# Optimization experiments

Hardware: AMD Instinct MI355X
Metric: run time of the kernel (lower is better)

The kernel has to match this reference:

```python
import jax, jax.numpy as jnp
import numpy as np

WS = 512   # window_size
LB = 1     # look_backward
LF = 1     # look_forward
H = 16     # num_attention_heads
NC = LB + LF + 1  # concatenated windows per query window


def _collect(a, pad_value):
    # a: [B, nw, ws, ...]; gather windows [i-LB, i+LF] for each window i,
    # padding the window axis with pad_value (faithful to collect_windows).
    nw = a.shape[1]
    pads = [(0, 0), (LB, LF)] + [(0, 0)] * (a.ndim - 2)
    ap = jnp.pad(a, pads, constant_values=pad_value)
    idx = jnp.arange(nw)[:, None] + jnp.arange(NC)[None, :]  # [nw, NC]
    g = ap[:, idx]  # [B, nw, NC, ws, ...]
    return g.reshape(g.shape[0], nw, NC * a.shape[2], *a.shape[3:])


def setup_inputs() -> dict:
    key = jax.random.key(0)
    ks = jax.random.split(key, 9)
    B, S, E = 1, 4096, 1024
    x = jax.random.normal(ks[0], (B, S, E), dtype=jnp.float32)
    std = 0.02
    wq = std * jax.random.normal(ks[1], (E, E), dtype=jnp.float32)
    wk = std * jax.random.normal(ks[2], (E, E), dtype=jnp.float32)
    wv = std * jax.random.normal(ks[3], (E, E), dtype=jnp.float32)
    wo = std * jax.random.normal(ks[4], (E, E), dtype=jnp.float32)
    bq = std * jax.random.normal(ks[5], (E,), dtype=jnp.float32)
    bk = std * jax.random.normal(ks[6], (E,), dtype=jnp.float32)
    bv = std * jax.random.normal(ks[7], (E,), dtype=jnp.float32)
    bo = std * jax.random.normal(ks[8], (E,), dtype=jnp.float32)
    return {"x": x, "wq": wq, "bq": bq, "wk": wk, "bk": bk,
            "wv": wv, "bv": bv, "wo": wo, "bo": bo}


def reference(x, wq, bq, wk, bk, wv, bv, wo, bo):
    B, S, E = x.shape
    hd = E // H
    nw = S // WS  # seq_len chosen divisible by window_size

    def proj(w, b):
        y = x @ w.T + b
        return y.reshape(B, S, H, hd).transpose(0, 2, 1, 3).reshape(B * H, S, hd)

    q = proj(wq, bq)
    k = proj(wk, bk)
    v = proj(wv, bv)

    qb = q.reshape(B * H, nw, WS, hd)
    # NOTE: original pads K/V window buffers with value -1 (not zero); pad
    # positions are NOT masked (the `!= -1` clause excludes them) -- replicated.
    kb = _collect(k.reshape(B * H, nw, WS, hd), -1.0)  # [BH, nw, NC*WS, hd]
    vb = _collect(v.reshape(B * H, nw, WS, hd), -1.0)

    t = jnp.arange(S, dtype=jnp.int32).reshape(1, nw, WS)
    ct = _collect(t, -1)  # [1, nw, NC*WS] key positions (-1 for pads)

    # Unscaled QK^T (original applies no 1/sqrt(d)).
    scores = jnp.einsum('bwqd,bwkd->bwqk', qb, kb)  # [BH, nw, WS, NC*WS]

    qi = t.reshape(1, nw, WS, 1)          # query absolute positions
    ctb = ct[:, :, None, :]               # key absolute positions
    over = ((ctb > qi + WS * LF) | (ctb < qi - WS * LB)) & (ctb != -1)
    scores = jnp.where(over, -jnp.inf, scores)

    attn = jax.nn.softmax(scores, axis=-1)
    out = jnp.einsum('bwqk,bwkd->bwqd', attn, vb)  # [BH, nw, WS, hd]
    out = out.reshape(B, H, S, hd).transpose(0, 2, 1, 3).reshape(B, S, E)
    return out @ wo.T + bo
```

## Files before the change

### kernel.cpp

```cpp
#include <hip/hip_runtime.h>
#include <stdint.h>

#define S 4096
#define E 1024
#define NH 16
#define HD 64
#define WSZ 512

typedef _Float16 f16x8 __attribute__((ext_vector_type(8)));
typedef _Float16 f16x4 __attribute__((ext_vector_type(4)));
typedef float f32x4 __attribute__((ext_vector_type(4)));
typedef unsigned short u16;
typedef unsigned int u32;

__device__ __forceinline__ u16 f2h_bits(float f) {
    union { _Float16 h; u16 u; } cv; cv.h = (_Float16)f; return cv.u;
}

__device__ __forceinline__ void gld16(const u16* g, u16* l) {
    __builtin_amdgcn_global_load_lds((const __attribute__((address_space(1))) void*)g,
                                     (__attribute__((address_space(3))) void*)l, 16, 0, 0);
}

struct CvtArgs {
    const float* s[5];
    u16* d[5];
    int n[5];
};
__global__ void cvt5(CvtArgs a) {
    int seg = blockIdx.y;
    const float* __restrict__ s = a.s[seg];
    u16* __restrict__ d = a.d[seg];
    int n = a.n[seg];
    for (int i = (blockIdx.x * 256 + threadIdx.x) * 4; i < n; i += gridDim.x * 1024) {
        float4 f = *(const float4*)&s[i];
        uint2 o;
        o.x = (u32)f2h_bits(f.x) | ((u32)f2h_bits(f.y) << 16);
        o.y = (u32)f2h_bits(f.z) | ((u32)f2h_bits(f.w) << 16);
        *(uint2*)&d[i] = o;
    }
}

__global__ __launch_bounds__(256) void gemm_qkv(
    const u16* __restrict__ A, const u16* __restrict__ B,
    u16* __restrict__ OutQK, u16* __restrict__ OutVT,
    const float* __restrict__ b0, const float* __restrict__ b1, const float* __restrict__ b2,
    int K) {
    __shared__ __align__(16) u16 As[128 * 32];
    __shared__ __align__(16) u16 Bs[128 * 32];
    const int tid = threadIdx.x;
    const int wid = tid >> 6, lid = tid & 63, quad = lid >> 4, l16 = lid & 15;
    const int wm = wid >> 1, wn = wid & 1;
    const int bm0 = blockIdx.x * 128, bn0 = blockIdx.y * 128;

    f32x4 acc[4][4] = {};
    const int sr = tid >> 2, sc = (tid & 3) * 8;

    for (int k0 = 0; k0 < K; k0 += 32) {
        __syncthreads();
        gld16(&A[(size_t)(bm0 + sr) * K + k0 + sc],      &As[tid * 8]);
        gld16(&A[(size_t)(bm0 + sr + 64) * K + k0 + sc], &As[2048 + tid * 8]);
        gld16(&B[(size_t)(bn0 + sr) * K + k0 + sc],      &Bs[tid * 8]);
        gld16(&B[(size_t)(bn0 + sr + 64) * K + k0 + sc], &Bs[2048 + tid * 8]);
        __syncthreads();
        f16x8 af[4], bf[4];
#pragma unroll
        for (int i = 0; i < 4; ++i) af[i] = *(const f16x8*)&As[(wm * 64 + i * 16 + l16) * 32 + quad * 8];
#pragma unroll
        for (int j = 0; j < 4; ++j) bf[j] = *(const f16x8*)&Bs[(wn * 64 + j * 16 + l16) * 32 + quad * 8];
#pragma unroll
        for (int i = 0; i < 4; ++i)
#pragma unroll
            for (int j = 0; j < 4; ++j)
                acc[i][j] = __builtin_amdgcn_mfma_f32_16x16x32_f16(af[i], bf[j], acc[i][j], 0, 0, 0);
    }

    const bool isV = (bn0 >= 2048);
#pragma unroll
    for (int j = 0; j < 4; ++j) {
        int n = bn0 + wn * 64 + j * 16 + l16;
        float bias = (n < 1024) ? b0[n] : (n < 2048 ? b1[n - 1024] : b2[n - 2048]);
#pragma unroll
        for (int i = 0; i < 4; ++i) {
            int m0 = bm0 + wm * 64 + i * 16 + quad * 4;
            if (!isV) {
#pragma unroll
                for (int r = 0; r < 4; ++r)
                    OutQK[(size_t)(m0 + r) * 2048 + n] = f2h_bits(acc[i][j][r] + bias);
            } else {
                u16 h0 = f2h_bits(acc[i][j][0] + bias);
                u16 h1 = f2h_bits(acc[i][j][1] + bias);
                u16 h2 = f2h_bits(acc[i][j][2] + bias);
                u16 h3 = f2h_bits(acc[i][j][3] + bias);
                uint2 pk;
                pk.x = (u32)h0 | ((u32)h1 << 16);
                pk.y = (u32)h2 | ((u32)h3 << 16);
                *(uint2*)&OutVT[(size_t)(n - 2048) * 4096 + m0] = pk;
            }
        }
    }
}

__global__ __launch_bounds__(256) void gemm_n64(
    const u16* __restrict__ A, const u16* __restrict__ B, float* __restrict__ OutF,
    const float* __restrict__ bias, int N, int K) {
    __shared__ __align__(16) u16 As[128 * 32];
    __shared__ __align__(16) u16 Bs[64 * 32];
    const int tid = threadIdx.x;
    const int wid = tid >> 6, lid = tid & 63, quad = lid >> 4, l16 = lid & 15;
    const int bm0 = blockIdx.x * 128, bn0 = blockIdx.y * 64;

    f32x4 acc[2][4] = {};
    const int sr = tid >> 2, sc = (tid & 3) * 8;

    for (int k0 = 0; k0 < K; k0 += 32) {
        __syncthreads();
        gld16(&A[(size_t)(bm0 + sr) * K + k0 + sc],      &As[tid * 8]);
        gld16(&A[(size_t)(bm0 + sr + 64) * K + k0 + sc], &As[2048 + tid * 8]);
        gld16(&B[(size_t)(bn0 + sr) * K + k0 + sc],      &Bs[tid * 8]);
        __syncthreads();
        f16x8 af[2], bf[4];
#pragma unroll
        for (int i = 0; i < 2; ++i) af[i] = *(const f16x8*)&As[(wid * 32 + i * 16 + l16) * 32 + quad * 8];
#pragma unroll
        for (int j = 0; j < 4; ++j) bf[j] = *(const f16x8*)&Bs[(j * 16 + l16) * 32 + quad * 8];
#pragma unroll
        for (int i = 0; i < 2; ++i)
#pragma unroll
            for (int j = 0; j < 4; ++j)
                acc[i][j] = __builtin_amdgcn_mfma_f32_16x16x32_f16(af[i], bf[j], acc[i][j], 0, 0, 0);
    }

#pragma unroll
    for (int j = 0; j < 4; ++j) {
        int n = bn0 + j * 16 + l16;
        float bv = bias[n];
#pragma unroll
        for (int i = 0; i < 2; ++i) {
            int m0 = bm0 + wid * 32 + i * 16 + quad * 4;
#pragma unroll
            for (int r = 0; r < 4; ++r)
                OutF[(size_t)(m0 + r) * N + n] = acc[i][j][r] + bv;
        }
    }
}

__global__ __launch_bounds__(512, 4) void attn_win(const u16* __restrict__ QK, const u16* __restrict__ VT,
                                                   u16* __restrict__ AO) {
    const int qt = blockIdx.x, w = blockIdx.y, h = blockIdx.z;
    const int tid = threadIdx.x, wid = tid >> 6, lid = tid & 63, quad = lid >> 4, l16 = lid & 15;

    __shared__ __align__(16) u16 Ks[2][2 * 64 * 32];
    __shared__ __align__(16) u16 Vt[2][2 * 64 * 36];

    const int qrow = w * WSZ + qt * 128 + wid * 16 + l16;
    const _Float16 L2E = (_Float16)1.44269504f;
    f16x8 qf[2];
#pragma unroll
    for (int ks = 0; ks < 2; ++ks) {
        qf[ks] = *(const f16x8*)&QK[(size_t)qrow * 2048 + h * 64 + ks * 32 + quad * 8];
#pragma unroll
        for (int j = 0; j < 8; ++j) qf[ks][j] *= L2E;
    }

    const int npad = (w == 0 || w == 7) ? 512 : 0;
    float s_p = 0.f;
    if (npad) {
        float sq = 0.f;
#pragma unroll
        for (int j = 0; j < 8; ++j) sq += (float)qf[0][j] + (float)qf[1][j];
        sq += __shfl_xor(sq, 16, 64);
        sq += __shfl_xor(sq, 32, 64);
        s_p = -sq;
    }

    f32x4 oacc[4] = {};
    float mrun = -30000.f;
    float lsum = 0.f;

    const int g0base = (w - 1) * WSZ;
    const int rqloc = qt * 128 + wid * 16 + l16;
    const int rqw0 = qt * 128 + wid * 16;

    int cfirst = 2 * qt; if ((1 - w) * 8 > cfirst) cfirst = (1 - w) * 8;
    int clast = 2 * qt + 17; if (71 - 8 * w < clast) clast = 71 - 8 * w; if (clast > 23) clast = 23;

    const int kst = tid & 255, kkh = tid >> 8;
    const int vd = tid >> 3, vk0 = (tid & 7) * 8;
    const size_t kgoff = 1024 + h * 64 + kkh * 32 + (kst & 3) * 8 + (size_t)(kst >> 2) * 2048;
    const int kloff = kkh * 2048 + kst * 8;
    const u16* vgrow = VT + (size_t)(h * 64 + vd) * 4096 + vk0;
    const int vloff = (vk0 >> 5) * 2304 + vd * 36 + (vk0 & 31);

    {
        const int g0 = g0base + cfirst * 64;
        uint4 va = *(const uint4*)(vgrow + g0);
        gld16(QK + (size_t)g0 * 2048 + kgoff, &Ks[0][0] + kloff);
        u16* vp = &Vt[0][0] + vloff;
        *(uint2*)(vp)     = make_uint2(va.x, va.y);
        *(uint2*)(vp + 4) = make_uint2(va.z, va.w);
    }

    int ib = 0;
    for (int c = cfirst; c <= clast; ++c, ib ^= 1) {
        __syncthreads();

        const bool has_next = (c < clast);
        uint4 vnext;
        if (has_next) {
            const int gn = g0base + (c + 1) * 64;
            vnext = *(const uint4*)(vgrow + gn);
            gld16(QK + (size_t)gn * 2048 + kgoff, &Ks[ib ^ 1][0] + kloff);
        }

        const u16* KsB = &Ks[ib][0];
        const u16* VtB = &Vt[ib][0];

        f32x4 sc[4];
#pragma unroll
        for (int nt = 0; nt < 4; ++nt) {
            f16x8 kf0 = *(const f16x8*)&KsB[(nt * 16 + l16) * 32 + quad * 8];
            f16x8 kf1 = *(const f16x8*)&KsB[2048 + (nt * 16 + l16) * 32 + quad * 8];
            f32x4 t = {};
            t = __builtin_amdgcn_mfma_f32_16x16x32_f16(kf0, qf[0], t, 0, 0, 0);
            t = __builtin_amdgcn_mfma_f32_16x16x32_f16(kf1, qf[1], t, 0, 0, 0);
            sc[nt] = t;
        }

        const bool needs_mask = (c * 64 < rqw0 + 16) || (c * 64 + 63 > rqw0 + 1024);
        if (needs_mask) {
#pragma unroll
            for (int nt = 0; nt < 4; ++nt)
#pragma unroll
                for (int r = 0; r < 4; ++r) {
                    int n = c * 64 + nt * 16 + quad * 4 + r;
                    if (n < rqloc || n > rqloc + 1024) sc[nt][r] = -30000.f;
                }
        }

        float mloc = mrun;
#pragma unroll
        for (int nt = 0; nt < 4; ++nt)
            mloc = fmaxf(mloc, fmaxf(fmaxf(sc[nt][0], sc[nt][1]), fmaxf(sc[nt][2], sc[nt][3])));
        mloc = fmaxf(mloc, __shfl_xor(mloc, 16, 64));
        mloc = fmaxf(mloc, __shfl_xor(mloc, 32, 64));

        const bool up = __any(mloc > mrun);
        float ls = 0.f;
        f16x4 pf[4];
#pragma unroll
        for (int nt = 0; nt < 4; ++nt)
#pragma unroll
            for (int r = 0; r < 4; ++r) {
                float p = exp2f(sc[nt][r] - mloc);
                ls += p;
                pf[nt][r] = (_Float16)p;
            }
        if (up) {
            float alpha = exp2f(mrun - mloc);
            mrun = mloc;
            lsum = lsum * alpha + ls;
            float ao[4];
#pragma unroll
            for (int r = 0; r < 4; ++r) ao[r] = __shfl(alpha, quad * 4 + r, 64);
#pragma unroll
            for (int dt = 0; dt < 4; ++dt)
#pragma unroll
                for (int r = 0; r < 4; ++r) oacc[dt][r] *= ao[r];
        } else {
            lsum += ls;
        }

#pragma unroll
        for (int nt = 0; nt < 4; ++nt)
#pragma unroll
            for (int dt = 0; dt < 4; ++dt) {
                f16x4 vf = *(const f16x4*)&VtB[(nt >> 1) * 2304 + (dt * 16 + l16) * 36 + (nt & 1) * 16 + quad * 4];
                oacc[dt] = __builtin_amdgcn_mfma_f32_16x16x16f16(pf[nt], vf, oacc[dt], 0, 0, 0);
            }

        if (has_next) {
            u16* vp = &Vt[ib ^ 1][0] + vloff;
            *(uint2*)(vp)     = make_uint2(vnext.x, vnext.y);
            *(uint2*)(vp + 4) = make_uint2(vnext.z, vnext.w);
        }
    }

    float lt = lsum;
    lt += __shfl_xor(lt, 16, 64);
    lt += __shfl_xor(lt, 32, 64);
    float aW = 1.f, pw = 0.f;
    if (npad) {
        float mnew = fmaxf(mrun, s_p);
        aW = exp2f(mrun - mnew);
        pw = 512.f * exp2f(s_p - mnew);
        lt = lt * aW + pw;
    }
    float linv = 1.f / lt;
    float lrec[4], arow[4], pwrow[4];
#pragma unroll
    for (int r = 0; r < 4; ++r) {
        lrec[r]  = __shfl(linv, quad * 4 + r, 64);
        arow[r]  = __shfl(aW,   quad * 4 + r, 64);
        pwrow[r] = __shfl(pw,   quad * 4 + r, 64);
    }
#pragma unroll
    for (int dt = 0; dt < 4; ++dt)
#pragma unroll
        for (int r = 0; r < 4; ++r) {
            int srow = w * WSZ + qt * 128 + wid * 16 + quad * 4 + r;
            int col = h * 64 + dt * 16 + l16;
            float o = (oacc[dt][r] * arow[r] - pwrow[r]) * lrec[r];
            AO[(size_t)srow * E + col] = f2h_bits(o);
        }
}

extern "C" void kernel_launch(void* const* d_in, const int* in_sizes, int n_in,
                              void* d_out, int out_size, void* d_ws, size_t ws_size,
                              hipStream_t stream) {
    const float* x  = (const float*)d_in[0];
    const float* wq = (const float*)d_in[1];
    const float* bq = (const float*)d_in[2];
    const float* wk = (const float*)d_in[3];
    const float* bk = (const float*)d_in[4];
    const float* wv = (const float*)d_in[5];
    const float* bv = (const float*)d_in[6];
    const float* wo = (const float*)d_in[7];
    const float* bo = (const float*)d_in[8];
    float* out = (float*)d_out;

    char* ws = (char*)d_ws;
    u16* XH  = (u16*)(ws);
    u16* WC  = (u16*)(ws + 8388608);
    u16* WOh = (u16*)(ws + 14680064);
    u16* QK  = (u16*)(ws + 16777216);
    u16* VTg = (u16*)(ws + 33554432);
    u16* AOh = (u16*)(ws + 41943040);

    CvtArgs ca;
    ca.s[0] = x;  ca.d[0] = XH;            ca.n[0] = 4194304;
    ca.s[1] = wq; ca.d[1] = WC;            ca.n[1] = 1048576;
    ca.s[2] = wk; ca.d[2] = WC + 1048576;  ca.n[2] = 1048576;
    ca.s[3] = wv; ca.d[3] = WC + 2097152;  ca.n[3] = 1048576;
    ca.s[4] = wo; ca.d[4] = WOh;           ca.n[4] = 1048576;
    cvt5<<<dim3(1024, 5), 256, 0, stream>>>(ca);

    gemm_qkv<<<dim3(32, 24), 256, 0, stream>>>(XH, WC, QK, VTg, bq, bk, bv, 1024);
    attn_win<<<dim3(4, 8, 16), 512, 0, stream>>>(QK, VTg, AOh);
    gemm_n64<<<dim3(32, 16), 256, 0, stream>>>(AOh, WOh, out, bo, 1024, 1024);
}
```

Baseline: 196.5 us.

## Deepen GEMM K-tiles to 64 and shrink attention blocks to 64 queries

Both projection GEMMs now stage a 64-wide K slice per iteration (two 32-wide halves in LDS), which halves the number of barrier pairs per tile and costs twice the shared memory. The attention kernel moves from 512-thread blocks covering 128 queries to 256-thread blocks covering 64 queries, and the grid doubles to compensate. Each thread now loads twice as much K/V per chunk. The smaller blocks give more of them for scheduling and better occupancy balance. In exchange, each K/V chunk is reused by fewer queries, so more K/V traffic is loaded redundantly across blocks.

```diff
diff --git a/kernel.cpp b/kernel.cpp
--- a/kernel.cpp
+++ b/kernel.cpp
@@ -46,33 +46,41 @@
     u16* __restrict__ OutQK, u16* __restrict__ OutVT,
     const float* __restrict__ b0, const float* __restrict__ b1, const float* __restrict__ b2,
     int K) {
-    __shared__ __align__(16) u16 As[128 * 32];
-    __shared__ __align__(16) u16 Bs[128 * 32];
+    __shared__ __align__(16) u16 As[2 * 128 * 32];
+    __shared__ __align__(16) u16 Bs[2 * 128 * 32];
     const int tid = threadIdx.x;
     const int wid = tid >> 6, lid = tid & 63, quad = lid >> 4, l16 = lid & 15;
     const int wm = wid >> 1, wn = wid & 1;
     const int bm0 = blockIdx.x * 128, bn0 = blockIdx.y * 128;
 
     f32x4 acc[4][4] = {};
-    const int sr = tid >> 2, sc = (tid & 3) * 8;
-
-    for (int k0 = 0; k0 < K; k0 += 32) {
-        __syncthreads();
-        gld16(&A[(size_t)(bm0 + sr) * K + k0 + sc],      &As[tid * 8]);
-        gld16(&A[(size_t)(bm0 + sr + 64) * K + k0 + sc], &As[2048 + tid * 8]);
-        gld16(&B[(size_t)(bn0 + sr) * K + k0 + sc],      &Bs[tid * 8]);
-        gld16(&B[(size_t)(bn0 + sr + 64) * K + k0 + sc], &Bs[2048 + tid * 8]);
-        __syncthreads();
-        f16x8 af[4], bf[4];
-#pragma unroll
-        for (int i = 0; i < 4; ++i) af[i] = *(const f16x8*)&As[(wm * 64 + i * 16 + l16) * 32 + quad * 8];
-#pragma unroll
-        for (int j = 0; j < 4; ++j) bf[j] = *(const f16x8*)&Bs[(wn * 64 + j * 16 + l16) * 32 + quad * 8];
-#pragma unroll
-        for (int i = 0; i < 4; ++i)
-#pragma unroll
-            for (int j = 0; j < 4; ++j)
-                acc[i][j] = __builtin_amdgcn_mfma_f32_16x16x32_f16(af[i], bf[j], acc[i][j], 0, 0, 0);
+    const int srow = tid >> 2, scol = (tid & 3) * 8;
+
+    for (int k0 = 0; k0 < K; k0 += 64) {
+        __syncthreads();
+#pragma unroll
+        for (int half = 0; half < 2; ++half)
+#pragma unroll
+            for (int rep = 0; rep < 2; ++rep) {
+                gld16(&A[(size_t)(bm0 + rep * 64 + srow) * K + k0 + half * 32 + scol],
+                      &As[half * 4096 + rep * 2048 + tid * 8]);
+                gld16(&B[(size_t)(bn0 + rep * 64 + srow) * K + k0 + half * 32 + scol],
+                      &Bs[half * 4096 + rep * 2048 + tid * 8]);
+            }
+        __syncthreads();
+#pragma unroll
+        for (int kk = 0; kk < 2; ++kk) {
+            f16x8 af[4], bf[4];
+#pragma unroll
+            for (int i = 0; i < 4; ++i) af[i] = *(const f16x8*)&As[kk * 4096 + (wm * 64 + i * 16 + l16) * 32 + quad * 8];
+#pragma unroll
+            for (int j = 0; j < 4; ++j) bf[j] = *(const f16x8*)&Bs[kk * 4096 + (wn * 64 + j * 16 + l16) * 32 + quad * 8];
+#pragma unroll
+            for (int i = 0; i < 4; ++i)
+#pragma unroll
+                for (int j = 0; j < 4; ++j)
+                    acc[i][j] = __builtin_amdgcn_mfma_f32_16x16x32_f16(af[i], bf[j], acc[i][j], 0, 0, 0);
+        }
     }
 
     const bool isV = (bn0 >= 2048);
@@ -104,31 +112,40 @@
 __global__ __launch_bounds__(256) void gemm_n64(
     const u16* __restrict__ A, const u16* __restrict__ B, float* __restrict__ OutF,
     const float* __restrict__ bias, int N, int K) {
-    __shared__ __align__(16) u16 As[128 * 32];
-    __shared__ __align__(16) u16 Bs[64 * 32];
+    __shared__ __align__(16) u16 As[2 * 128 * 32];
+    __shared__ __align__(16) u16 Bs[2 * 64 * 32];
     const int tid = threadIdx.x;
     const int wid = tid >> 6, lid = tid & 63, quad = lid >> 4, l16 = lid & 15;
     const int bm0 = blockIdx.x * 128, bn0 = blockIdx.y * 64;
 
     f32x4 acc[2][4] = {};
-    const int sr = tid >> 2, sc = (tid & 3) * 8;
-
-    for (int k0 = 0; k0 < K; k0 += 32) {
-        __syncthreads();
-        gld16(&A[(size_t)(bm0 + sr) * K + k0 + sc],      &As[tid * 8]);
-        gld16(&A[(size_t)(bm0 + sr + 64) * K + k0 + sc], &As[2048 + tid * 8]);
-        gld16(&B[(size_t)(bn0 + sr) * K + k0 + sc],      &Bs[tid * 8]);
-        __syncthreads();
-        f16x8 af[2], bf[4];
-#pragma unroll
-        for (int i = 0; i < 2; ++i) af[i] = *(const f16x8*)&As[(wid * 32 + i * 16 + l16) * 32 + quad * 8];
-#pragma unroll
-        for (int j = 0; j < 4; ++j) bf[j] = *(const f16x8*)&Bs[(j * 16 + l16) * 32 + quad * 8];
-#pragma unroll
-        for (int i = 0; i < 2; ++i)
-#pragma unroll
-            for (int j = 0; j < 4; ++j)
-                acc[i][j] = __builtin_amdgcn_mfma_f32_16x16x32_f16(af[i], bf[j], acc[i][j], 0, 0, 0);
+    const int srow = tid >> 2, scol = (tid & 3) * 8;
+
+    for (int k0 = 0; k0 < K; k0 += 64) {
+        __syncthreads();
+#pragma unroll
+        for (int half = 0; half < 2; ++half) {
+#pragma unroll
+            for (int rep = 0; rep < 2; ++rep)
+                gld16(&A[(size_t)(bm0 + rep * 64 + srow) * K + k0 + half * 32 + scol],
+                      &As[half * 4096 + rep * 2048 + tid * 8]);
+            gld16(&B[(size_t)(bn0 + srow) * K + k0 + half * 32 + scol],
+                  &Bs[half * 2048 + tid * 8]);
+        }
+        __syncthreads();
+#pragma unroll
+        for (int kk = 0; kk < 2; ++kk) {
+            f16x8 af[2], bf[4];
+#pragma unroll
+            for (int i = 0; i < 2; ++i) af[i] = *(const f16x8*)&As[kk * 4096 + (wid * 32 + i * 16 + l16) * 32 + quad * 8];
+#pragma unroll
+            for (int j = 0; j < 4; ++j) bf[j] = *(const f16x8*)&Bs[kk * 2048 + (j * 16 + l16) * 32 + quad * 8];
+#pragma unroll
+            for (int i = 0; i < 2; ++i)
+#pragma unroll
+                for (int j = 0; j < 4; ++j)
+                    acc[i][j] = __builtin_amdgcn_mfma_f32_16x16x32_f16(af[i], bf[j], acc[i][j], 0, 0, 0);
+        }
     }
 
 #pragma unroll
@@ -145,15 +162,15 @@
     }
 }
 
-__global__ __launch_bounds__(512, 4) void attn_win(const u16* __restrict__ QK, const u16* __restrict__ VT,
-                                                   u16* __restrict__ AO) {
+__global__ __launch_bounds__(256) void attn_win(const u16* __restrict__ QK, const u16* __restrict__ VT,
+                                                u16* __restrict__ AO) {
     const int qt = blockIdx.x, w = blockIdx.y, h = blockIdx.z;
     const int tid = threadIdx.x, wid = tid >> 6, lid = tid & 63, quad = lid >> 4, l16 = lid & 15;
 
     __shared__ __align__(16) u16 Ks[2][2 * 64 * 32];
     __shared__ __align__(16) u16 Vt[2][2 * 64 * 36];
 
-    const int qrow = w * WSZ + qt * 128 + wid * 16 + l16;
+    const int qrow = w * WSZ + qt * 64 + wid * 16 + l16;
     const _Float16 L2E = (_Float16)1.44269504f;
     f16x8 qf[2];
 #pragma unroll
@@ -179,26 +196,29 @@
     float lsum = 0.f;
 
     const int g0base = (w - 1) * WSZ;
-    const int rqloc = qt * 128 + wid * 16 + l16;
-    const int rqw0 = qt * 128 + wid * 16;
-
-    int cfirst = 2 * qt; if ((1 - w) * 8 > cfirst) cfirst = (1 - w) * 8;
-    int clast = 2 * qt + 17; if (71 - 8 * w < clast) clast = 71 - 8 * w; if (clast > 23) clast = 23;
-
-    const int kst = tid & 255, kkh = tid >> 8;
-    const int vd = tid >> 3, vk0 = (tid & 7) * 8;
-    const size_t kgoff = 1024 + h * 64 + kkh * 32 + (kst & 3) * 8 + (size_t)(kst >> 2) * 2048;
-    const int kloff = kkh * 2048 + kst * 8;
+    const int rqloc = qt * 64 + wid * 16 + l16;
+    const int rqw0 = qt * 64 + wid * 16;
+
+    int cfirst = qt; if ((1 - w) * 8 > cfirst) cfirst = (1 - w) * 8;
+    int clast = qt + 16; if (71 - 8 * w < clast) clast = 71 - 8 * w; if (clast > 23) clast = 23;
+
+    const size_t kgoff = 1024 + h * 64 + (tid & 3) * 8 + (size_t)(tid >> 2) * 2048;
+    const int kl = tid * 8;
+    const int vd = tid >> 2, vk0 = (tid & 3) * 16;
     const u16* vgrow = VT + (size_t)(h * 64 + vd) * 4096 + vk0;
     const int vloff = (vk0 >> 5) * 2304 + vd * 36 + (vk0 & 31);
 
     {
         const int g0 = g0base + cfirst * 64;
         uint4 va = *(const uint4*)(vgrow + g0);
-        gld16(QK + (size_t)g0 * 2048 + kgoff, &Ks[0][0] + kloff);
+        uint4 vb = *(const uint4*)(vgrow + g0 + 8);
+        gld16(QK + (size_t)g0 * 2048 + kgoff, &Ks[0][0] + kl);
+        gld16(QK + (size_t)g0 * 2048 + kgoff + 32, &Ks[0][0] + 2048 + kl);
         u16* vp = &Vt[0][0] + vloff;
-        *(uint2*)(vp)     = make_uint2(va.x, va.y);
-        *(uint2*)(vp + 4) = make_uint2(va.z, va.w);
+        *(uint2*)(vp)      = make_uint2(va.x, va.y);
+        *(uint2*)(vp + 4)  = make_uint2(va.z, va.w);
+        *(uint2*)(vp + 8)  = make_uint2(vb.x, vb.y);
+        *(uint2*)(vp + 12) = make_uint2(vb.z, vb.w);
     }
 
     int ib = 0;
@@ -206,11 +226,13 @@
         __syncthreads();
 
         const bool has_next = (c < clast);
-        uint4 vnext;
+        uint4 vna, vnb;
         if (has_next) {
             const int gn = g0base + (c + 1) * 64;
-            vnext = *(const uint4*)(vgrow + gn);
-            gld16(QK + (size_t)gn * 2048 + kgoff, &Ks[ib ^ 1][0] + kloff);
+            vna = *(const uint4*)(vgrow + gn);
+            vnb = *(const uint4*)(vgrow + gn + 8);
+            gld16(QK + (size_t)gn * 2048 + kgoff, &Ks[ib ^ 1][0] + kl);
+            gld16(QK + (size_t)gn * 2048 + kgoff + 32, &Ks[ib ^ 1][0] + 2048 + kl);
         }
 
         const u16* KsB = &Ks[ib][0];
@@ -281,8 +303,10 @@
 
         if (has_next) {
             u16* vp = &Vt[ib ^ 1][0] + vloff;
-            *(uint2*)(vp)     = make_uint2(vnext.x, vnext.y);
-            *(uint2*)(vp + 4) = make_uint2(vnext.z, vnext.w);
+            *(uint2*)(vp)      = make_uint2(vna.x, vna.y);
+            *(uint2*)(vp + 4)  = make_uint2(vna.z, vna.w);
+            *(uint2*)(vp + 8)  = make_uint2(vnb.x, vnb.y);
+            *(uint2*)(vp + 12) = make_uint2(vnb.z, vnb.w);
         }
     }
 
@@ -308,7 +332,7 @@
     for (int dt = 0; dt < 4; ++dt)
 #pragma unroll
         for (int r = 0; r < 4; ++r) {
-            int srow = w * WSZ + qt * 128 + wid * 16 + quad * 4 + r;
+            int srow = w * WSZ + qt * 64 + wid * 16 + quad * 4 + r;
             int col = h * 64 + dt * 16 + l16;
             float o = (oacc[dt][r] * arow[r] - pwrow[r]) * lrec[r];
             AO[(size_t)srow * E + col] = f2h_bits(o);
@@ -346,6 +370,6 @@
     cvt5<<<dim3(1024, 5), 256, 0, stream>>>(ca);
 
     gemm_qkv<<<dim3(32, 24), 256, 0, stream>>>(XH, WC, QK, VTg, bq, bk, bv, 1024);
-    attn_win<<<dim3(4, 8, 16), 512, 0, stream>>>(QK, VTg, AOh);
+    attn_win<<<dim3(8, 8, 16), 256, 0, stream>>>(QK, VTg, AOh);
     gemm_n64<<<dim3(32, 16), 256, 0, stream>>>(AOh, WOh, out, bo, 1024, 1024);
 }
```

Result: no change. 196.8 us (+0.1%).
